# Performance work log

Hardware: AMD Instinct MI355X
Metric: run time of the kernel (lower is better)

## Reference

```python
import jax, jax.numpy as jnp
import numpy as np
import math

EPS = 1.1920929e-07  # torch.finfo(float32).eps, used by nn.RMSNorm(eps=None)

def rmsnorm(x, w):
    return x * jax.lax.rsqrt(jnp.mean(x * x, axis=-1, keepdims=True) + EPS) * w

def sinkhorn(logits, iters=20):
    m = jnp.exp(logits - logits.max(axis=-1, keepdims=True))
    def body(_, m):
        m = m / (m.sum(axis=-1, keepdims=True) + 1e-6)
        return m / (m.sum(axis=-2, keepdims=True) + 1e-6)
    return jax.lax.fori_loop(0, iters, body, m)

def ngram_hash(ids, mults):
    # ids [B,T] int32, mults [2,2,3] int32 -> [B,T,4]
    B, T = ids.shape
    padded = jnp.pad(ids, ((0, 0), (2, 0)))
    windows = jnp.stack([padded[:, k:k + T] for k in range(3)], axis=-1)  # [B,T,3]
    out = []
    for n_idx in range(2):
        L = n_idx + 2
        grams = windows[:, :, 3 - L:]                                     # [B,T,L]
        mixed = grams[:, :, None, :] * mults[n_idx, :, :L][None, None]    # [B,T,2,L]
        h = mixed[..., 0]
        for k in range(1, L):
            h = jnp.bitwise_xor(h, mixed[..., k])
        out.append(h % 4096)
    return jnp.concatenate(out, axis=2)

def short_conv(x, conv_w, norm_w):
    # depthwise causal conv, kernel 4: torch pads 3 both sides then slices [..., :T]
    B, T, G, C = x.shape
    xn = rmsnorm(x, norm_w).reshape(B, T, G * C).transpose(0, 2, 1)  # [B,GC,T]
    y = jax.lax.conv_general_dilated(xn, conv_w, (1,), [(3, 0)],
                                     feature_group_count=G * C,
                                     dimension_numbers=('NCH', 'OIH', 'NCH'))
    return jax.nn.silu(y).transpose(0, 2, 1).reshape(B, T, G, C)

def engram(x, ids, mults, emb_table, val_w, val_b, key_w, key_b, nq_w, nk_w, conv_w, convnorm_w):
    B, T = ids.shape
    hash_ids = ngram_hash(ids, mults) + jnp.array([0, 4096, 8192, 12288], dtype=jnp.int32)
    emb = emb_table[hash_ids].reshape(B, T, -1)                       # [B,T,256]
    v_base = emb @ val_w + val_b                                      # [B,T,128]
    k = rmsnorm(jnp.einsum('btd,sdc->btsc', emb, key_w) + key_b, nk_w)  # [B,T,4,128]
    q = rmsnorm(x, nq_w)
    gates = jax.nn.sigmoid(jnp.sum(q * k, axis=-1, keepdims=True) / math.sqrt(128.0))
    v_gated = v_base[:, :, None, :] * gates                           # [B,T,4,128]
    return v_gated + short_conv(v_gated, conv_w, convnorm_w)

def causal_attn(x, qkv_w, qkv_b, proj_w, proj_b):
    B, T, C = x.shape
    H, D = 4, C // 4
    q, k, v = jnp.split(x @ qkv_w + qkv_b, 3, axis=-1)
    q = q.reshape(B, T, H, D).transpose(0, 2, 1, 3)
    k = k.reshape(B, T, H, D).transpose(0, 2, 1, 3)
    v = v.reshape(B, T, H, D).transpose(0, 2, 1, 3)
    att = jnp.einsum('bhtd,bhsd->bhts', q, k) / math.sqrt(D)
    att = jnp.where(jnp.tril(jnp.ones((T, T), bool)), att, -jnp.inf)
    att = jax.nn.softmax(att, axis=-1)
    y = jnp.einsum('bhts,bhsd->bhtd', att, v).transpose(0, 2, 1, 3).reshape(B, T, C)
    return y @ proj_w + proj_b

def mhc(x, layer_fn, coef_w, pre_w, pre_b, post_w, post_b, res_w, res_b, a_pre, a_post, a_res, ln_w):
    B, T, n, C = x.shape
    xn = rmsnorm(x.reshape(B * T, n * C), coef_w)
    H_pre = jax.nn.sigmoid(a_pre * (xn @ pre_w + pre_b))             # [BT,n]
    H_post = 2.0 * jax.nn.sigmoid(a_post * (xn @ post_w + post_b))   # [BT,n]
    H_res = sinkhorn((a_res * (xn @ res_w + res_b)).reshape(-1, n, n))
    xp = x.reshape(B * T, n, C)
    x_agg = jnp.einsum('bn,bnc->bc', H_pre, xp)
    y = layer_fn(rmsnorm(x_agg.reshape(B, T, C), ln_w)).reshape(B * T, C)
    # faithful to torch einsum 'bjn,bc->bnc' applied to H_post.transpose(1,2) [BT,n,1]:
    # the stream dim j is CONTRACTED, leaving a size-1 dim that broadcasts over streams
    x_branch = H_post.sum(axis=-1)[:, None, None] * y[:, None, :]    # [BT,1,C]
    x_highway = jnp.einsum('bnm,bmc->bnc', H_res, xp)                # [BT,n,C]
    return (x_highway + x_branch).reshape(B, T, n, C)

def _forward(x, input_ids, eng_multipliers, eng_embedding, eng_val_w, eng_val_b, eng_key_w, eng_key_b, eng_nq_w, eng_nk_w, eng_conv_w, eng_convnorm_w, a_coef_w, a_pre_w, a_pre_b, a_post_w, a_post_b, a_res_w, a_res_b, a_alpha_pre, a_alpha_post, a_alpha_res, a_ln_w, qkv_w, qkv_b, attnproj_w, attnproj_b, m_coef_w, m_pre_w, m_pre_b, m_post_w, m_post_b, m_res_w, m_res_b, m_alpha_pre, m_alpha_post, m_alpha_res, m_ln_w, mlp_w1, mlp_b1, mlp_w2, mlp_b2):
    x = x + engram(x, input_ids, eng_multipliers, eng_embedding, eng_val_w, eng_val_b, eng_key_w, eng_key_b, eng_nq_w, eng_nk_w, eng_conv_w, eng_convnorm_w)
    attn_fn = lambda z: causal_attn(z, qkv_w, qkv_b, attnproj_w, attnproj_b)
    x = mhc(x, attn_fn, a_coef_w, a_pre_w, a_pre_b, a_post_w, a_post_b, a_res_w, a_res_b, a_alpha_pre, a_alpha_post, a_alpha_res, a_ln_w)
    mlp_fn = lambda z: jax.nn.silu(z @ mlp_w1 + mlp_b1) @ mlp_w2 + mlp_b2
    x = mhc(x, mlp_fn, m_coef_w, m_pre_w, m_pre_b, m_post_w, m_post_b, m_res_w, m_res_b, m_alpha_pre, m_alpha_post, m_alpha_res, m_ln_w)
    return x

def setup_inputs():
    key = jax.random.key(0)
    B, T = 256, 128
    def rnd(i, shp, scale=0.02):
        return jax.random.normal(jax.random.fold_in(key, i), shp, jnp.float32) * scale
    alpha = jnp.asarray(0.01, jnp.float32)
    return {
        'x': rnd(0, (B, T, 4, 128), 1.0),
        'input_ids': jax.random.randint(jax.random.fold_in(key, 1), (B, T), 0, 4096, jnp.int32),
        'eng_multipliers': jax.random.randint(jax.random.fold_in(key, 2), (2, 2, 3), 1, 10000, jnp.int32),
        'eng_embedding': rnd(3, (16384, 64)),
        'eng_val_w': rnd(4, (256, 128)), 'eng_val_b': jnp.zeros(128, jnp.float32),
        'eng_key_w': rnd(5, (4, 256, 128)), 'eng_key_b': jnp.zeros((4, 128), jnp.float32),
        'eng_nq_w': jnp.ones((4, 128), jnp.float32), 'eng_nk_w': jnp.ones((4, 128), jnp.float32),
        'eng_conv_w': rnd(6, (512, 1, 4), 0.1), 'eng_convnorm_w': jnp.ones((4, 128), jnp.float32),
        'a_coef_w': jnp.ones(512, jnp.float32),
        'a_pre_w': rnd(7, (512, 4)), 'a_pre_b': jnp.zeros(4, jnp.float32),
        'a_post_w': rnd(8, (512, 4)), 'a_post_b': jnp.zeros(4, jnp.float32),
        'a_res_w': rnd(9, (512, 16)), 'a_res_b': jnp.zeros(16, jnp.float32),
        'a_alpha_pre': alpha, 'a_alpha_post': alpha, 'a_alpha_res': alpha,
        'a_ln_w': jnp.ones(128, jnp.float32),
        'qkv_w': rnd(10, (128, 384)), 'qkv_b': jnp.zeros(384, jnp.float32),
        'attnproj_w': rnd(11, (128, 128)), 'attnproj_b': jnp.zeros(128, jnp.float32),
        'm_coef_w': jnp.ones(512, jnp.float32),
        'm_pre_w': rnd(12, (512, 4)), 'm_pre_b': jnp.zeros(4, jnp.float32),
        'm_post_w': rnd(13, (512, 4)), 'm_post_b': jnp.zeros(4, jnp.float32),
        'm_res_w': rnd(14, (512, 16)), 'm_res_b': jnp.zeros(16, jnp.float32),
        'm_alpha_pre': alpha, 'm_alpha_post': alpha, 'm_alpha_res': alpha,
        'm_ln_w': jnp.ones(128, jnp.float32),
        'mlp_w1': rnd(15, (128, 512)), 'mlp_b1': jnp.zeros(512, jnp.float32),
        'mlp_w2': rnd(16, (512, 128)), 'mlp_b2': jnp.zeros(128, jnp.float32),
    }

def reference(x, input_ids, eng_multipliers, eng_embedding, eng_val_w, eng_val_b, eng_key_w, eng_key_b, eng_nq_w, eng_nk_w, eng_conv_w, eng_convnorm_w, a_coef_w, a_pre_w, a_pre_b, a_post_w, a_post_b, a_res_w, a_res_b, a_alpha_pre, a_alpha_post, a_alpha_res, a_ln_w, qkv_w, qkv_b, attnproj_w, attnproj_b, m_coef_w, m_pre_w, m_pre_b, m_post_w, m_post_b, m_res_w, m_res_b, m_alpha_pre, m_alpha_post, m_alpha_res, m_ln_w, mlp_w1, mlp_b1, mlp_w2, mlp_b2):
    return _forward(x, input_ids, eng_multipliers, eng_embedding, eng_val_w, eng_val_b, eng_key_w, eng_key_b, eng_nq_w, eng_nk_w, eng_conv_w, eng_convnorm_w, a_coef_w, a_pre_w, a_pre_b, a_post_w, a_post_b, a_res_w, a_res_b, a_alpha_pre, a_alpha_post, a_alpha_res, a_ln_w, qkv_w, qkv_b, attnproj_w, attnproj_b, m_coef_w, m_pre_w, m_pre_b, m_post_w, m_post_b, m_res_w, m_res_b, m_alpha_pre, m_alpha_post, m_alpha_res, m_ln_w, mlp_w1, mlp_b1, mlp_w2, mlp_b2)
```

## Files before the change

### kernel.cpp

```cpp
#include <hip/hip_runtime.h>

#define BT 32768
#define TSEQ 128

constexpr float EPSF = 1.1920929e-07f;

typedef __attribute__((ext_vector_type(8))) short bf16x8;
typedef __attribute__((ext_vector_type(4))) float f32x4;

__device__ __forceinline__ float sigm(float z) { return 1.f / (1.f + __expf(-z)); }

__device__ __forceinline__ short bf16c(float f) {
  union { float f; unsigned u; } v; v.f = f;
  unsigned r = v.u + 0x7FFFu + ((v.u >> 16) & 1u);
  return (short)(r >> 16);
}
__device__ __forceinline__ float bf2f(short s) {
  union { unsigned u; float f; } v; v.u = ((unsigned)(unsigned short)s) << 16;
  return v.f;
}

__device__ __forceinline__ float red64(float v) {
  v += __shfl_xor(v, 1);  v += __shfl_xor(v, 2);  v += __shfl_xor(v, 4);
  v += __shfl_xor(v, 8);  v += __shfl_xor(v, 16); v += __shfl_xor(v, 32);
  return v;
}
__device__ __forceinline__ float red16(float v) {
  v += __shfl_xor(v, 1); v += __shfl_xor(v, 2); v += __shfl_xor(v, 4); v += __shfl_xor(v, 8);
  return v;
}
__device__ __forceinline__ float redmax16(float v) {
  v = fmaxf(v, __shfl_xor(v, 1)); v = fmaxf(v, __shfl_xor(v, 2));
  v = fmaxf(v, __shfl_xor(v, 4)); v = fmaxf(v, __shfl_xor(v, 8));
  return v;
}
__device__ __forceinline__ void load8(float* d, const float* p) {
  const float4 a = *reinterpret_cast<const float4*>(p);
  const float4 b = *reinterpret_cast<const float4*>(p + 4);
  d[0]=a.x; d[1]=a.y; d[2]=a.z; d[3]=a.w; d[4]=b.x; d[5]=b.y; d[6]=b.z; d[7]=b.w;
}

__global__ __launch_bounds__(256) void prep(
    const float* __restrict__ qkv_w, const float* __restrict__ proj_w,
    const float* __restrict__ mlp_w1, const float* __restrict__ mlp_w2,
    const float* __restrict__ val_w, const float* __restrict__ key_w,
    const float* __restrict__ a_res_w, const float* __restrict__ a_pre_w,
    const float* __restrict__ a_post_w,
    const float* __restrict__ m_res_w, const float* __restrict__ m_pre_w,
    const float* __restrict__ m_post_w,
    const float* __restrict__ a_res_b, const float* __restrict__ a_pre_b,
    const float* __restrict__ a_post_b,
    const float* __restrict__ m_res_b, const float* __restrict__ m_pre_b,
    const float* __restrict__ m_post_b,
    short* __restrict__ wt_qkv, short* __restrict__ wt_proj,
    short* __restrict__ wt_mlp1, short* __restrict__ wt_mlp2,
    short* __restrict__ wt_eng, short* __restrict__ wpk_a,
    short* __restrict__ wpk_m, float* __restrict__ bpk_a,
// ... 93 lines not shown
    for (int ks = 0; ks < 2; ++ks) {
      const int slot = ks * 4 + kg;
      bf16x8 af[2], bft;
#pragma unroll
      for (int mi = 0; mi < 2; ++mi) {
        const int r = wm * 32 + mi * 16 + lr;
        af[mi] = *reinterpret_cast<const bf16x8*>(&As[r * 64 + ((slot ^ (r & 7)) << 3)]);
      }
      {
        const int rb = wn * 16 + lr;
        bft = *reinterpret_cast<const bf16x8*>(&Bs[rb * 64 + ((slot ^ (rb & 7)) << 3)]);
      }
#pragma unroll
      for (int mi = 0; mi < 2; ++mi)
        acc[mi] = __builtin_amdgcn_mfma_f32_16x16x32_bf16(af[mi], bft, acc[mi], 0, 0, 0);
    }
  }
#pragma unroll
  for (int mi = 0; mi < 2; ++mi) {
    const int col = wn * 16 + lr;
    const float bv = bias[col];
#pragma unroll
    for (int j = 0; j < 4; ++j) {
      const int row = i0 + wm * 32 + mi * 16 + kg * 4 + j;
      out[(size_t)row * 32 + col] = acc[mi][j] + bv;
    }
  }
}

__global__ __launch_bounds__(256) void eng_mgemm(
    const int* __restrict__ ids, const int* __restrict__ mults,
    const float* __restrict__ table, const float* __restrict__ val_b,
    const short* __restrict__ wt_eng,
    float* __restrict__ vbase, float* __restrict__ kraw)
{
  __shared__ int hid[128][4];
  __shared__ short As[128 * 64];
  __shared__ short Bs[128 * 64];
  const int tid = threadIdx.x;
  const int i0 = blockIdx.x * 128;
  const int by = blockIdx.y;
  const int c0 = by * 128;
#pragma unroll
  for (int p = 0; p < 2; ++p) {
    const int idx = tid + p * 256;
    const int r = idx >> 2, wh = idx & 3;
    const int i = i0 + r;
    const int b = i >> 7, tt = i & 127;
    const int* __restrict__ row = ids + b * TSEQ;
    const int g2 = row[tt];
    const int g1 = (tt >= 1) ? row[tt - 1] : 0;
    const int g0 = (tt >= 2) ? row[tt - 2] : 0;
    int h;
    if (wh == 0)      h = ((g1 * mults[0]) ^ (g2 * mults[1])) & 4095;
    else if (wh == 1) h = (((g1 * mults[3]) ^ (g2 * mults[4])) & 4095) + 4096;
    else if (wh == 2) h = (((g0 * mults[6]) ^ (g1 * mults[7]) ^ (g2 * mults[8])) & 4095) + 8192;
    else              h = (((g0 * mults[9]) ^ (g1 * mults[10]) ^ (g2 * mults[11])) & 4095) + 12288;
    hid[r][wh] = h;
  }
  const int w = tid >> 6, l = tid & 63;
  const int wr = (w >> 1) * 64, wc = (w & 1) * 64;
  f32x4 acc[4][4];
#pragma unroll
  for (int mi = 0; mi < 4; ++mi)
#pragma unroll
    for (int ni = 0; ni < 4; ++ni) acc[mi][ni] = {0.f, 0.f, 0.f, 0.f};

// ... 22 lines not shown
#pragma unroll
    for (int ks = 0; ks < 2; ++ks) {
      const int slot = ks * 4 + kg;
      bf16x8 af[4], bft[4];
#pragma unroll
      for (int mi = 0; mi < 4; ++mi) {
        const int r = wr + mi * 16 + lr;
        af[mi] = *reinterpret_cast<const bf16x8*>(&As[r * 64 + ((slot ^ (r & 7)) << 3)]);
      }
#pragma unroll
      for (int ni = 0; ni < 4; ++ni) {
        const int r = wc + ni * 16 + lr;
        bft[ni] = *reinterpret_cast<const bf16x8*>(&Bs[r * 64 + ((slot ^ (r & 7)) << 3)]);
      }
#pragma unroll
      for (int mi = 0; mi < 4; ++mi)
#pragma unroll
        for (int ni = 0; ni < 4; ++ni)
          acc[mi][ni] = __builtin_amdgcn_mfma_f32_16x16x32_bf16(af[mi], bft[ni], acc[mi][ni], 0, 0, 0);
    }
  }
  const int lr = l & 15, hi = l >> 4;
#pragma unroll
  for (int mi = 0; mi < 4; ++mi)
#pragma unroll
    for (int ni = 0; ni < 4; ++ni) {
      const int col = wc + ni * 16 + lr;
#pragma unroll
      for (int j = 0; j < 4; ++j) {
        const int row = i0 + wr + mi * 16 + hi * 4 + j;
        if (by == 0)
          vbase[(size_t)row * 128 + col] = acc[mi][ni][j] + val_b[col];
        else
          kraw[(size_t)row * 512 + (by - 1) * 128 + col] = acc[mi][ni][j];
      }
    }
}

__global__ __launch_bounds__(512) void fused_gateconv(
    const float* __restrict__ kraw, const float* __restrict__ x,
    const float* __restrict__ vbase, const float* __restrict__ key_b,
    const float* __restrict__ nk_w, const float* __restrict__ nq_w,
    const float* __restrict__ conv_w, const float* __restrict__ cnw,
    float* __restrict__ xout, float* __restrict__ invout)
{
  __shared__ float vb[128 * 128];
  __shared__ float gA[128][4];
  __shared__ float gG[128][4];
  __shared__ float prt[128][2];
  const int tid = threadIdx.x;
  const size_t rowbase = (size_t)blockIdx.x * 128;
#pragma unroll
  for (int p = 0; p < 8; ++p) {
    const int idx = p * 512 + tid;
    *reinterpret_cast<float4*>(&vb[idx * 4]) =
        *reinterpret_cast<const float4*>(vbase + rowbase * 128 + (size_t)idx * 4);
  }
  __syncthreads();
  const int w = tid >> 6, l = tid & 63;
  {
    const int s = l >> 4, li = l & 15, c0 = li * 8, j0 = l * 8;
    float kb[8], nk[8], nq[8];
    load8(kb, key_b + s * 128 + c0);
    load8(nk, nk_w + s * 128 + c0);
    load8(nq, nq_w + s * 128 + c0);
    for (int it = 0; it < 16; ++it) {
      const int t = w * 16 + it;
      const size_t rg = rowbase + t;
      float kv[8], xv[8];
      load8(kv, kraw + rg * 512 + j0);
      load8(xv, x + rg * 512 + j0);
      float ssk = 0.f, ssx = 0.f;
#pragma unroll
      for (int jj = 0; jj < 8; ++jj) {
        kv[jj] += kb[jj];
        ssk = fmaf(kv[jj], kv[jj], ssk);
        ssx = fmaf(xv[jj], xv[jj], ssx);
      }
      ssk = red16(ssk);
      ssx = red16(ssx);
      const float invk = rsqrtf(ssk * (1.f / 128.f) + EPSF);
      const float invq = rsqrtf(ssx * (1.f / 128.f) + EPSF);
      float dot = 0.f;
#pragma unroll
      for (int jj = 0; jj < 8; ++jj)
        dot = fmaf(kv[jj] * invk * nk[jj], xv[jj] * invq * nq[jj], dot);
      dot = red16(dot);
      const float gate = sigm(dot * 0.08838834764831843f);
      const float2 vb2 = *reinterpret_cast<const float2*>(&vb[t * 128 + l * 2]);
      float ssv = vb2.x * vb2.x + vb2.y * vb2.y;
      ssv = red64(ssv);
      const float A = gate * rsqrtf(gate * gate * (ssv * (1.f / 128.f)) + EPSF);
      if (li == 0) { gG[t][s] = gate; gA[t][s] = A; }
    }
  }
  __syncthreads();
  {
    const int cg = tid >> 7;
    const int cjf = (tid & 127) * 4;
    const int cjh = cjf & 127;
    const int sj = cjf >> 7;
    float4 cwe[4];
#pragma unroll
    for (int e = 0; e < 4; ++e)
      cwe[e] = *reinterpret_cast<const float4*>(conv_w + (size_t)(cjf + e) * 4);
    const float4 cn4 = *reinterpret_cast<const float4*>(cnw + cjf);
    for (int tt = 0; tt < 32; ++tt) {
      const int t = tt * 4 + cg;
      float4 vbt[4]; float av[4];
#pragma unroll
      for (int kk = 0; kk < 4; ++kk) {
        const int t2 = t - 3 + kk;
        if (t2 >= 0) {
          vbt[kk] = *reinterpret_cast<const float4*>(&vb[t2 * 128 + cjh]);
          av[kk] = gA[t2][sj];
        } else {
          vbt[kk] = make_float4(0.f, 0.f, 0.f, 0.f);
          av[kk] = 0.f;
        }
      }
      float4 accv;
      accv.x = vbt[0].x*av[0]*cwe[0].x + vbt[1].x*av[1]*cwe[0].y + vbt[2].x*av[2]*cwe[0].z + vbt[3].x*av[3]*cwe[0].w;
      accv.y = vbt[0].y*av[0]*cwe[1].x + vbt[1].y*av[1]*cwe[1].y + vbt[2].y*av[2]*cwe[1].z + vbt[3].y*av[3]*cwe[1].w;
      accv.z = vbt[0].z*av[0]*cwe[2].x + vbt[1].z*av[1]*cwe[2].y + vbt[2].z*av[2]*cwe[2].z + vbt[3].z*av[3]*cwe[2].w;
      accv.w = vbt[0].w*av[0]*cwe[3].x + vbt[1].w*av[1]*cwe[3].y + vbt[2].w*av[2]*cwe[3].z + vbt[3].w*av[3]*cwe[3].w;
      const float4 x4 = *reinterpret_cast<const float4*>(x + (rowbase + t) * 512 + cjf);
      const float gg = gG[t][sj];
      float4 o;
      const float y0 = accv.x * cn4.x, y1 = accv.y * cn4.y;
      const float y2 = accv.z * cn4.z, y3 = accv.w * cn4.w;
      o.x = x4.x + vbt[3].x * gg + y0 * sigm(y0);
      o.y = x4.y + vbt[3].y * gg + y1 * sigm(y1);
      o.z = x4.z + vbt[3].z * gg + y2 * sigm(y2);
      o.w = x4.w + vbt[3].w * gg + y3 * sigm(y3);
      *reinterpret_cast<float4*>(xout + (rowbase + t) * 512 + cjf) = o;
      float ssq = o.x*o.x + o.y*o.y + o.z*o.z + o.w*o.w;
      ssq = red64(ssq);
      if (l == 0) prt[t][(tid >> 6) & 1] = ssq;
    }
  }
  __syncthreads();
  if (tid < 128)
    invout[rowbase + tid] = rsqrtf((prt[tid][0] + prt[tid][1]) * (1.f / 512.f) + EPSF);
}

__global__ __launch_bounds__(256) void mhc_sink2(
    const float* __restrict__ proj, const float* __restrict__ xin,
    const float* __restrict__ p_apre, const float* __restrict__ p_apost,
    const float* __restrict__ p_ares, const float* __restrict__ ln_w,
    unsigned short* __restrict__ xab, float* __restrict__ hres,
    float* __restrict__ hps)
{
  const int tid = threadIdx.x;
  const int l = tid & 63;
  const size_t i = (size_t)blockIdx.x * 4 + (tid >> 6);
  const float pv = proj[i * 32 + (l & 31)];
  const float apre = p_apre[0], apost = p_apost[0], ares = p_ares[0];
  const int n = l >> 4;
  const float hp = sigm(apre * __shfl(pv, 16 + n));
  float hsum = 0.f;
#pragma unroll
  for (int t2 = 0; t2 < 4; ++t2) hsum += 2.f * sigm(apost * __shfl(pv, 20 + t2));
  const float v = ares * pv;
  float rm = fmaxf(v, __shfl_xor(v, 1));
  rm = fmaxf(rm, __shfl_xor(rm, 2));
  float m = __expf(v - rm);
#pragma unroll
  for (int it = 0; it < 20; ++it) {
    float rs = m + __shfl_xor(m, 1);
    rs += __shfl_xor(rs, 2);
    m *= __builtin_amdgcn_rcpf(rs + 1e-6f);
    float cs = m + __shfl_xor(m, 4);
    cs += __shfl_xor(cs, 8);
    m *= __builtin_amdgcn_rcpf(cs + 1e-6f);
  }
  if (l < 16) hres[i * 16 + l] = m;
  if (l == 0) hps[i] = hsum;
  const int j0 = l * 8;
  float xv[8];
  load8(xv, xin + i * 512 + j0);
  float ag[8];
#pragma unroll
  for (int jj = 0; jj < 8; ++jj) {
    float a2 = hp * xv[jj];
    a2 += __shfl_xor(a2, 16);
    a2 += __shfl_xor(a2, 32);
    ag[jj] = a2;
  }
  float ssa = 0.f;
#pragma unroll
  for (int jj = 0; jj < 8; ++jj) ssa = fmaf(ag[jj], ag[jj], ssa);
  ssa = red16(ssa);
  const float inva = rsqrtf(ssa * (1.f / 128.f) + EPSF);
  if (l < 16) {
    float lnw[8];
    load8(lnw, ln_w + l * 8);
    bf16x8 o;
#pragma unroll
    for (int jj = 0; jj < 8; ++jj) o[jj] = bf16c(ag[jj] * inva * lnw[jj]);
    *reinterpret_cast<bf16x8*>(xab + i * 128 + l * 8) = o;
  }
}

template <int NT, int ACT>
__global__ __launch_bounds__(256) void mgemm_bf16A(
    const unsigned short* __restrict__ Ab, const short* __restrict__ WT,
    const float* __restrict__ bias, float* __restrict__ outp)
{
  __shared__ short As[128 * 64];
  __shared__ short Bs[128 * 64];
  const int tid = threadIdx.x;
  const int i0 = blockIdx.x * 128;
  const int c0 = blockIdx.y * 128;
  const int w = tid >> 6, l = tid & 63;
  const int wr = (w >> 1) * 64, wc = (w & 1) * 64;
  const int kg = l >> 4, lr = l & 15;
  f32x4 acc[4][4];
#pragma unroll
  for (int mi = 0; mi < 4; ++mi)
#pragma unroll
    for (int ni = 0; ni < 4; ++ni) acc[mi][ni] = {0.f, 0.f, 0.f, 0.f};

#pragma unroll
  for (int kc = 0; kc < 2; ++kc) {
    __syncthreads();
#pragma unroll
    for (int p = 0; p < 4; ++p) {
      const int idx = p * 256 + tid;
      const int r = idx >> 3, slb = idx & 7;
      const bf16x8 v = *reinterpret_cast<const bf16x8*>(Ab + (size_t)(i0 + r) * 128 + kc * 64 + slb * 8);
      *reinterpret_cast<bf16x8*>(&As[r * 64 + ((slb ^ (r & 7)) << 3)]) = v;
    }
#pragma unroll
    for (int p = 0; p < 4; ++p) {
      const int idx = p * 256 + tid;
      const int r = idx >> 3, slb = idx & 7;
      const bf16x8 v = *reinterpret_cast<const bf16x8*>(WT + (size_t)(c0 + r) * 128 + kc * 64 + slb * 8);
      *reinterpret_cast<bf16x8*>(&Bs[r * 64 + ((slb ^ (r & 7)) << 3)]) = v;
    }
    __syncthreads();
#pragma unroll
    for (int ks = 0; ks < 2; ++ks) {
      const int slot = ks * 4 + kg;
      bf16x8 af[4], bft[4];
#pragma unroll
      for (int mi = 0; mi < 4; ++mi) {
        const int r = wr + mi * 16 + lr;
        af[mi] = *reinterpret_cast<const bf16x8*>(&As[r * 64 + ((slot ^ (r & 7)) << 3)]);
      }
#pragma unroll
      for (int ni = 0; ni < 4; ++ni) {
        const int r = wc + ni * 16 + lr;
        bft[ni] = *reinterpret_cast<const bf16x8*>(&Bs[r * 64 + ((slot ^ (r & 7)) << 3)]);
      }
#pragma unroll
      for (int mi = 0; mi < 4; ++mi)
#pragma unroll
        for (int ni = 0; ni < 4; ++ni)
          acc[mi][ni] = __builtin_amdgcn_mfma_f32_16x16x32_bf16(af[mi], bft[ni], acc[mi][ni], 0, 0, 0);
    }
  }
#pragma unroll
  for (int mi = 0; mi < 4; ++mi)
#pragma unroll
    for (int ni = 0; ni < 4; ++ni) {
      const int col = c0 + wc + ni * 16 + lr;
      const float bv = bias[col];
#pragma unroll
      for (int j = 0; j < 4; ++j) {
        const int row = i0 + wr + mi * 16 + kg * 4 + j;
        float o = acc[mi][ni][j] + bv;
        if (ACT == 1) o = o * sigm(o);
        outp[(size_t)row * (NT * 128) + col] = o;
      }
    }
}

template <int KT, bool WITH_INV>
__global__ __launch_bounds__(512) void gemm_combine(
    const float* __restrict__ A, const int lda,
    const short* __restrict__ WT, const float* __restrict__ bias,
    const float* __restrict__ xst, const float* __restrict__ hres,
    const float* __restrict__ hps, float* __restrict__ outp,
    float* __restrict__ invout)
{
  __shared__ short As[128 * 64];
  __shared__ short Bs[128 * 64];
  __shared__ short yl[128 * 132];
  __shared__ float prt[128][2];
  const int tid = threadIdx.x;
  const size_t i0 = (size_t)blockIdx.x * 128;
  const int w = tid >> 6, l = tid & 63;
  const int wm = w >> 2, wn = w & 3;
  const int kg = l >> 4, lr = l & 15;
  f32x4 acc[4][2];
#pragma unroll
  for (int mi = 0; mi < 4; ++mi)
#pragma unroll
    for (int ni = 0; ni < 2; ++ni) acc[mi][ni] = {0.f, 0.f, 0.f, 0.f};
#pragma unroll
  for (int kc = 0; kc < KT; ++kc) {
    __syncthreads();
#pragma unroll
    for (int p = 0; p < 4; ++p) {
      const int idx = p * 512 + tid;
      const int r = idx >> 4, c4 = idx & 15;
      const float4 v = *reinterpret_cast<const float4*>(A + (i0 + r) * lda + kc * 64 + c4 * 4);
      short4 b4; b4.x = bf16c(v.x); b4.y = bf16c(v.y); b4.z = bf16c(v.z); b4.w = bf16c(v.w);
      *reinterpret_cast<short4*>(&As[r * 64 + (((c4 >> 1) ^ (r & 7)) << 3) + ((c4 & 1) << 2)]) = b4;
    }
#pragma unroll
    for (int p = 0; p < 2; ++p) {
      const int idx = p * 512 + tid;
      const int r = idx >> 3, slb = idx & 7;
      const bf16x8 v = *reinterpret_cast<const bf16x8*>(
          WT + (size_t)r * (KT * 64) + kc * 64 + slb * 8);
      *reinterpret_cast<bf16x8*>(&Bs[r * 64 + ((slb ^ (r & 7)) << 3)]) = v;
    }
    __syncthreads();
#pragma unroll
    for (int ks = 0; ks < 2; ++ks) {
      const int slot = ks * 4 + kg;
      bf16x8 af[4], bft[2];
#pragma unroll
      for (int mi = 0; mi < 4; ++mi) {
        const int r = wm * 64 + mi * 16 + lr;
        af[mi] = *reinterpret_cast<const bf16x8*>(&As[r * 64 + ((slot ^ (r & 7)) << 3)]);
      }
#pragma unroll
      for (int ni = 0; ni < 2; ++ni) {
        const int rb = wn * 32 + ni * 16 + lr;
        bft[ni] = *reinterpret_cast<const bf16x8*>(&Bs[rb * 64 + ((slot ^ (rb & 7)) << 3)]);
      }
#pragma unroll
      for (int mi = 0; mi < 4; ++mi)
#pragma unroll
        for (int ni = 0; ni < 2; ++ni)
          acc[mi][ni] = __builtin_amdgcn_mfma_f32_16x16x32_bf16(af[mi], bft[ni], acc[mi][ni], 0, 0, 0);
    }
  }
#pragma unroll
  for (int mi = 0; mi < 4; ++mi)
#pragma unroll
    for (int ni = 0; ni < 2; ++ni) {
      const int col = wn * 32 + ni * 16 + lr;
      const float bv = bias[col];
#pragma unroll
      for (int j = 0; j < 4; ++j) {
        const int row = wm * 64 + mi * 16 + kg * 4 + j;
        yl[row * 132 + col] = bf16c(acc[mi][ni][j] + bv);
      }
    }
  __syncthreads();
  const int c = tid & 127, tl = tid >> 7;
  for (int k = 0; k < 32; ++k) {
    const int t = tl * 32 + k;
    const size_t rg = i0 + t;
    float hv[16];
#pragma unroll
    for (int n16 = 0; n16 < 16; ++n16) hv[n16] = hres[rg * 16 + n16];
    const float g = hps[rg];
    const float yv = bf2f(yl[t * 132 + c]) * g;
    float xm[4];
#pragma unroll
    for (int m = 0; m < 4; ++m) xm[m] = xst[rg * 512 + m * 128 + c];
    float ssq = 0.f;
#pragma unroll
    for (int n = 0; n < 4; ++n) {
      const float o = hv[n*4+0]*xm[0] + hv[n*4+1]*xm[1] + hv[n*4+2]*xm[2] + hv[n*4+3]*xm[3] + yv;
      outp[rg * 512 + n * 128 + c] = o;
      if (WITH_INV) ssq = fmaf(o, o, ssq);
    }
    if (WITH_INV) {
      ssq = red64(ssq);
      if (l == 0) prt[t][(tid >> 6) & 1] = ssq;
    }
  }
  if (WITH_INV) {
    __syncthreads();
    if (tid < 128)
      invout[i0 + tid] = rsqrtf((prt[tid][0] + prt[tid][1]) * (1.f / 512.f) + EPSF);
  }
}

__global__ __launch_bounds__(256) void attn_mfma(
    const float* __restrict__ qkv, float* __restrict__ y)
{
  __shared__ short Ks[128 * 32];
  __shared__ short Vt[32 * 128];
  __shared__ short Ps[4][32 * 128];
  const int tid = threadIdx.x;
  const int b = blockIdx.x >> 2, h = blockIdx.x & 3;
  const float* __restrict__ base = qkv + (size_t)b * 128 * 384 + h * 32;
#pragma unroll
  for (int p = 0; p < 4; ++p) {
    const int idx = tid + p * 256;
    const int s = idx >> 3, c4 = idx & 7;
    const float4 v = *reinterpret_cast<const float4*>(base + (size_t)s * 384 + 128 + c4 * 4);
    short4 o; o.x = bf16c(v.x); o.y = bf16c(v.y); o.z = bf16c(v.z); o.w = bf16c(v.w);
    const int chunk = (c4 >> 1) ^ ((s >> 1) & 3);
    *reinterpret_cast<short4*>(&Ks[s * 32 + chunk * 8 + (c4 & 1) * 4]) = o;
  }
#pragma unroll
  for (int p = 0; p < 4; ++p) {
    const int idx = tid + p * 256;
    const int s = idx >> 3, c4 = idx & 7;
    const float4 v = *reinterpret_cast<const float4*>(base + (size_t)s * 384 + 256 + c4 * 4);
    const int schunk = s >> 3, soff = s & 7;
#pragma unroll
    for (int k = 0; k < 4; ++k) {
      const int d = c4 * 4 + k;
      const float vv = (k == 0) ? v.x : (k == 1) ? v.y : (k == 2) ? v.z : v.w;
      Vt[d * 128 + ((schunk ^ (d & 7)) << 3) + soff] = bf16c(vv);
    }
  }
  const int w = tid >> 6, l = tid & 63;
  const int g = l >> 4, lr = l & 15;
  bf16x8 qa[2];
#pragma unroll
  for (int mi = 0; mi < 2; ++mi) {
    const int row = w * 32 + mi * 16 + lr;
    const float* qp = base + (size_t)row * 384 + g * 8;
    const float4 a = *reinterpret_cast<const float4*>(qp);
    const float4 c = *reinterpret_cast<const float4*>(qp + 4);
    bf16x8 q;
    q[0] = bf16c(a.x); q[1] = bf16c(a.y); q[2] = bf16c(a.z); q[3] = bf16c(a.w);
    q[4] = bf16c(c.x); q[5] = bf16c(c.y); q[6] = bf16c(c.z); q[7] = bf16c(c.w);
    qa[mi] = q;
  }
  __syncthreads();
  const int ntmax = 2 * w + 1;
  bf16x8 ka[8];
#pragma unroll
  for (int nt = 0; nt < 8; ++nt)
    if (nt <= ntmax) {
      const int s = nt * 16 + lr;
      const int chunk = g ^ ((s >> 1) & 3);
      ka[nt] = *reinterpret_cast<const bf16x8*>(&Ks[s * 32 + chunk * 8]);
    }
  f32x4 sacc[2][8];
#pragma unroll
  for (int mi = 0; mi < 2; ++mi)
#pragma unroll
    for (int nt = 0; nt < 8; ++nt) sacc[mi][nt] = {0.f, 0.f, 0.f, 0.f};
#pragma unroll
  for (int mi = 0; mi < 2; ++mi)
#pragma unroll
    for (int nt = 0; nt < 8; ++nt)
      if (nt <= ntmax)
        sacc[mi][nt] = __builtin_amdgcn_mfma_f32_16x16x32_bf16(qa[mi], ka[nt], sacc[mi][nt], 0, 0, 0);
  const float scl = 0.17677669529663687f;
  float rv[2][4];
  short* const pw = Ps[w];
#pragma unroll
  for (int mi = 0; mi < 2; ++mi) {
#pragma unroll
    for (int j = 0; j < 4; ++j) {
      const int row = w * 32 + mi * 16 + g * 4 + j;
      float mx = -3.4e38f;
#pragma unroll
      for (int nt = 0; nt < 8; ++nt)
// ... 23 lines not shown
#pragma unroll
  for (int mi = 0; mi < 2; ++mi)
#pragma unroll
    for (int nt = 0; nt < 2; ++nt) oacc[mi][nt] = {0.f, 0.f, 0.f, 0.f};
#pragma unroll
  for (int kt = 0; kt < 4; ++kt)
    if (kt <= w) {
      bf16x8 pa[2], va[2];
#pragma unroll
      for (int mi = 0; mi < 2; ++mi) {
        const int rl = mi * 16 + lr;
        const int chunk = (4 * kt + g) ^ (rl & 7);
        pa[mi] = *reinterpret_cast<const bf16x8*>(&pw[rl * 128 + chunk * 8]);
      }
#pragma unroll
      for (int nt = 0; nt < 2; ++nt) {
        const int d = nt * 16 + lr;
        const int chunk = (4 * kt + g) ^ (d & 7);
        va[nt] = *reinterpret_cast<const bf16x8*>(&Vt[d * 128 + chunk * 8]);
      }
#pragma unroll
      for (int mi = 0; mi < 2; ++mi)
#pragma unroll
        for (int nt = 0; nt < 2; ++nt)
          oacc[mi][nt] = __builtin_amdgcn_mfma_f32_16x16x32_bf16(pa[mi], va[nt], oacc[mi][nt], 0, 0, 0);
    }
#pragma unroll
  for (int mi = 0; mi < 2; ++mi)
#pragma unroll
    for (int nt = 0; nt < 2; ++nt)
#pragma unroll
      for (int j = 0; j < 4; ++j) {
        const int row = w * 32 + mi * 16 + g * 4 + j;
        y[((size_t)b * 128 + row) * 128 + h * 32 + nt * 16 + lr] = oacc[mi][nt][j] * rv[mi][j];
      }
}

extern "C" void kernel_launch(void* const* d_in, const int* in_sizes, int n_in,
                              void* d_out, int out_size, void* d_ws, size_t ws_size,
                              hipStream_t stream)
{
  const float* x        = (const float*)d_in[0];
  const int*   ids      = (const int*)d_in[1];
  const int*   mults    = (const int*)d_in[2];
  const float* table    = (const float*)d_in[3];
  const float* val_w    = (const float*)d_in[4];
  const float* val_b    = (const float*)d_in[5];
  const float* key_w    = (const float*)d_in[6];
  const float* key_b    = (const float*)d_in[7];
  const float* nq_w     = (const float*)d_in[8];
  const float* nk_w     = (const float*)d_in[9];
  const float* conv_w   = (const float*)d_in[10];
  const float* cnw      = (const float*)d_in[11];
  const float* a_coef   = (const float*)d_in[12];
  const float* a_pre_w  = (const float*)d_in[13];
  const float* a_pre_b  = (const float*)d_in[14];
  const float* a_post_w = (const float*)d_in[15];
  const float* a_post_b = (const float*)d_in[16];
  const float* a_res_w  = (const float*)d_in[17];
  const float* a_res_b  = (const float*)d_in[18];
  const float* a_apre   = (const float*)d_in[19];
  const float* a_apost  = (const float*)d_in[20];
  const float* a_ares   = (const float*)d_in[21];
  const float* a_ln_w   = (const float*)d_in[22];
  const float* qkv_w    = (const float*)d_in[23];
  const float* qkv_b    = (const float*)d_in[24];
  const float* proj_w   = (const float*)d_in[25];
  const float* proj_b   = (const float*)d_in[26];
  const float* m_coef   = (const float*)d_in[27];
  const float* m_pre_w  = (const float*)d_in[28];
  const float* m_pre_b  = (const float*)d_in[29];
  const float* m_post_w = (const float*)d_in[30];
  const float* m_post_b = (const float*)d_in[31];
  const float* m_res_w  = (const float*)d_in[32];
  const float* m_res_b  = (const float*)d_in[33];
  const float* m_apre   = (const float*)d_in[34];
  const float* m_apost  = (const float*)d_in[35];
  const float* m_ares   = (const float*)d_in[36];
  const float* m_ln_w   = (const float*)d_in[37];
  const float* mlp_w1   = (const float*)d_in[38];
  const float* mlp_b1   = (const float*)d_in[39];
  const float* mlp_w2   = (const float*)d_in[40];
  const float* mlp_b2   = (const float*)d_in[41];

  float* out = (float*)d_out;
  float* ws  = (float*)d_ws;
  float* vbase = ws;
  float* kraw  = vbase + (size_t)BT * 128;
  float* y1    = kraw  + (size_t)BT * 512;
  float* hresb = y1    + (size_t)BT * 128;
  float* hpsb  = hresb + (size_t)BT * 16;
  float* inv1  = hpsb  + (size_t)BT;
  float* inv2  = inv1  + (size_t)BT;
  float* bpk_a = inv2  + (size_t)BT;
  float* bpk_m = bpk_a + 32;
  short* wt_qkv  = (short*)(bpk_m + 32);
  short* wt_proj = wt_qkv  + 49152;
  short* wt_mlp1 = wt_proj + 16384;
  short* wt_mlp2 = wt_mlp1 + 65536;
  short* wt_eng  = wt_mlp2 + 65536;
  short* wpk_a   = wt_eng  + 163840;
  short* wpk_m   = wpk_a   + 16384;
  unsigned short* xab = (unsigned short*)(wpk_m + 16384);
  float* proj24  = y1;

  prep<<<1537, 256, 0, stream>>>(qkv_w, proj_w, mlp_w1, mlp_w2, val_w, key_w,
                                 a_res_w, a_pre_w, a_post_w, m_res_w, m_pre_w, m_post_w,
                                 a_res_b, a_pre_b, a_post_b, m_res_b, m_pre_b, m_post_b,
                                 wt_qkv, wt_proj, wt_mlp1, wt_mlp2, wt_eng,
                                 wpk_a, wpk_m, bpk_a, bpk_m);

  eng_mgemm<<<dim3(BT / 128, 5), 256, 0, stream>>>(ids, mults, table, val_b, wt_eng,
                                                   vbase, kraw);
  fused_gateconv<<<256, 512, 0, stream>>>(kraw, x, vbase, key_b, nk_w, nq_w,
                                          conv_w, cnw, out, inv1);

  mgemm32<<<BT / 64, 256, 0, stream>>>(out, 512, wpk_a, bpk_a, proj24, 512, inv1, a_coef);
  mhc_sink2<<<BT / 4, 256, 0, stream>>>(proj24, out, a_apre, a_apost, a_ares, a_ln_w,
                                        xab, hresb, hpsb);
  mgemm_bf16A<3, 0><<<dim3(BT / 128, 3), 256, 0, stream>>>(xab, wt_qkv, qkv_b, kraw);
  attn_mfma<<<1024, 256, 0, stream>>>(kraw, y1);
  gemm_combine<2, true><<<256, 512, 0, stream>>>(y1, 128, wt_proj, proj_b,
                                                 out, hresb, hpsb, kraw, inv2);

  mgemm32<<<BT / 64, 256, 0, stream>>>(kraw, 512, wpk_m, bpk_m, proj24, 512, inv2, m_coef);
  mhc_sink2<<<BT / 4, 256, 0, stream>>>(proj24, kraw, m_apre, m_apost, m_ares, m_ln_w,
                                        xab, hresb, hpsb);
  mgemm_bf16A<4, 1><<<dim3(BT / 128, 4), 256, 0, stream>>>(xab, wt_mlp1, mlp_b1, out);
  gemm_combine<8, false><<<256, 512, 0, stream>>>(out, 512, wt_mlp2, mlp_b2,
                                                  kraw, hresb, hpsb, out, nullptr);

  (void)in_sizes; (void)n_in; (void)out_size; (void)ws_size;
}
```

Baseline: 313.9 us.

## Store intermediates as bf16 and shrink gateconv/combine tiles for more blocks

Intermediate activations (engram keys, qkv, attention output, MLP hidden) are now written as bf16 instead of fp32. Consumers load them directly without converting, which roughly halves the global memory traffic between kernels. fused_gateconv now processes 32 rows per block with a 3-row halo instead of 128 rows, and gemm_combine uses 64-row tiles, so both launch many more blocks. The trade-off is recomputing the gates on halo rows, extra rounding of keys to bf16 before the RMSNorm, and a rearranged workspace with aliased buffers.

```diff
diff --git a/kernel.cpp b/kernel.cpp
--- a/kernel.cpp
+++ b/kernel.cpp
@@ -23,6 +23,11 @@
 __device__ __forceinline__ float red64(float v) {
   v += __shfl_xor(v, 1);  v += __shfl_xor(v, 2);  v += __shfl_xor(v, 4);
   v += __shfl_xor(v, 8);  v += __shfl_xor(v, 16); v += __shfl_xor(v, 32);
+  return v;
+}
+__device__ __forceinline__ float red32(float v) {
+  v += __shfl_xor(v, 1); v += __shfl_xor(v, 2); v += __shfl_xor(v, 4);
+  v += __shfl_xor(v, 8); v += __shfl_xor(v, 16);
   return v;
 }
 __device__ __forceinline__ float red16(float v) {
@@ -182,7 +187,7 @@
     const int* __restrict__ ids, const int* __restrict__ mults,
     const float* __restrict__ table, const float* __restrict__ val_b,
     const short* __restrict__ wt_eng,
-    float* __restrict__ vbase, float* __restrict__ kraw)
+    float* __restrict__ vbase, unsigned short* __restrict__ krawb)
 {
   __shared__ int hid[128][4];
   __shared__ short As[128 * 64];
@@ -271,29 +276,35 @@
         if (by == 0)
           vbase[(size_t)row * 128 + col] = acc[mi][ni][j] + val_b[col];
         else
-          kraw[(size_t)row * 512 + (by - 1) * 128 + col] = acc[mi][ni][j];
-      }
-    }
-}
-
-__global__ __launch_bounds__(512) void fused_gateconv(
-    const float* __restrict__ kraw, const float* __restrict__ x,
+          krawb[(size_t)row * 512 + (by - 1) * 128 + col] =
+              (unsigned short)bf16c(acc[mi][ni][j]);
+      }
+    }
+}
+
+__global__ __launch_bounds__(256) void fused_gateconv(
+    const unsigned short* __restrict__ krawb, const float* __restrict__ x,
     const float* __restrict__ vbase, const float* __restrict__ key_b,
     const float* __restrict__ nk_w, const float* __restrict__ nq_w,
     const float* __restrict__ conv_w, const float* __restrict__ cnw,
     float* __restrict__ xout, float* __restrict__ invout)
 {
-  __shared__ float vb[128 * 128];
-  __shared__ float gA[128][4];
-  __shared__ float gG[128][4];
-  __shared__ float prt[128][2];
+  __shared__ float vb[35 * 128];
+  __shared__ float gA[35][4];
+  __shared__ float gG[35][4];
   const int tid = threadIdx.x;
-  const size_t rowbase = (size_t)blockIdx.x * 128;
-#pragma unroll
-  for (int p = 0; p < 8; ++p) {
-    const int idx = p * 512 + tid;
-    *reinterpret_cast<float4*>(&vb[idx * 4]) =
-        *reinterpret_cast<const float4*>(vbase + rowbase * 128 + (size_t)idx * 4);
+  const size_t rowbase = (size_t)blockIdx.x * 32;
+  const int tt0 = (int)(rowbase & 127);
+#pragma unroll
+  for (int p = 0; p < 5; ++p) {
+    const int idx = p * 256 + tid;
+    if (idx < 1120) {
+      const int hs = idx >> 5, c4 = (idx & 31) << 2;
+      float4 v = make_float4(0.f, 0.f, 0.f, 0.f);
+      if (tt0 - 3 + hs >= 0)
+        v = *reinterpret_cast<const float4*>(vbase + (rowbase - 3 + hs) * 128 + c4);
+      *reinterpret_cast<float4*>(&vb[hs * 128 + c4]) = v;
+    }
   }
   __syncthreads();
   const int w = tid >> 6, l = tid & 63;
@@ -303,11 +314,21 @@
     load8(kb, key_b + s * 128 + c0);
     load8(nk, nk_w + s * 128 + c0);
     load8(nq, nq_w + s * 128 + c0);
-    for (int it = 0; it < 16; ++it) {
-      const int t = w * 16 + it;
-      const size_t rg = rowbase + t;
+    for (int it = 0; it < 9; ++it) {
+      const int ht = it * 4 + w;
+      if (ht >= 35) break;
+      const int tt = tt0 - 3 + ht;
+      if (tt < 0) {
+        if (li == 0) { gG[ht][s] = 0.f; gA[ht][s] = 0.f; }
+        continue;
+      }
+      const size_t rg = rowbase - 3 + ht;
       float kv[8], xv[8];
-      load8(kv, kraw + rg * 512 + j0);
+      {
+        const bf16x8 kvb = *reinterpret_cast<const bf16x8*>(krawb + rg * 512 + j0);
+#pragma unroll
+        for (int jj = 0; jj < 8; ++jj) kv[jj] = bf2f(kvb[jj]);
+      }
       load8(xv, x + rg * 512 + j0);
       float ssk = 0.f, ssx = 0.f;
 #pragma unroll
@@ -326,61 +347,57 @@
         dot = fmaf(kv[jj] * invk * nk[jj], xv[jj] * invq * nq[jj], dot);
       dot = red16(dot);
       const float gate = sigm(dot * 0.08838834764831843f);
-      const float2 vb2 = *reinterpret_cast<const float2*>(&vb[t * 128 + l * 2]);
+      const float2 vb2 = *reinterpret_cast<const float2*>(&vb[ht * 128 + l * 2]);
       float ssv = vb2.x * vb2.x + vb2.y * vb2.y;
       ssv = red64(ssv);
       const float A = gate * rsqrtf(gate * gate * (ssv * (1.f / 128.f)) + EPSF);
-      if (li == 0) { gG[t][s] = gate; gA[t][s] = A; }
+      if (li == 0) { gG[ht][s] = gate; gA[ht][s] = A; }
     }
   }
   __syncthreads();
   {
-    const int cg = tid >> 7;
-    const int cjf = (tid & 127) * 4;
-    const int cjh = cjf & 127;
-    const int sj = cjf >> 7;
-    float4 cwe[4];
-#pragma unroll
-    for (int e = 0; e < 4; ++e)
-      cwe[e] = *reinterpret_cast<const float4*>(conv_w + (size_t)(cjf + e) * 4);
-    const float4 cn4 = *reinterpret_cast<const float4*>(cnw + cjf);
-    for (int tt = 0; tt < 32; ++tt) {
-      const int t = tt * 4 + cg;
-      float4 vbt[4]; float av[4];
-#pragma unroll
-      for (int kk = 0; kk < 4; ++kk) {
-        const int t2 = t - 3 + kk;
-        if (t2 >= 0) {
-          vbt[kk] = *reinterpret_cast<const float4*>(&vb[t2 * 128 + cjh]);
-          av[kk] = gA[t2][sj];
-        } else {
-          vbt[kk] = make_float4(0.f, 0.f, 0.f, 0.f);
-          av[kk] = 0.f;
+    const int tg = tid >> 5;
+    const int c4l = tid & 31;
+    const int cf = c4l * 4;
+    for (int ti = 0; ti < 4; ++ti) {
+      const int t = tg + ti * 8;
+      const size_t rg = rowbase + t;
+      float ssq = 0.f;
+#pragma unroll
+      for (int sj = 0; sj < 4; ++sj) {
+        const int j = sj * 128 + cf;
+        float4 cwe[4];
+#pragma unroll
+        for (int e = 0; e < 4; ++e)
+          cwe[e] = *reinterpret_cast<const float4*>(conv_w + (size_t)(j + e) * 4);
+        const float4 cn4 = *reinterpret_cast<const float4*>(cnw + j);
+        float4 vbt[4]; float av[4];
+#pragma unroll
+        for (int kk = 0; kk < 4; ++kk) {
+          vbt[kk] = *reinterpret_cast<const float4*>(&vb[(t + kk) * 128 + cf]);
+          av[kk] = gA[t + kk][sj];
         }
-      }
-      float4 accv;
-      accv.x = vbt[0].x*av[0]*cwe[0].x + vbt[1].x*av[1]*cwe[0].y + vbt[2].x*av[2]*cwe[0].z + vbt[3].x*av[3]*cwe[0].w;
-      accv.y = vbt[0].y*av[0]*cwe[1].x + vbt[1].y*av[1]*cwe[1].y + vbt[2].y*av[2]*cwe[1].z + vbt[3].y*av[3]*cwe[1].w;
-      accv.z = vbt[0].z*av[0]*cwe[2].x + vbt[1].z*av[1]*cwe[2].y + vbt[2].z*av[2]*cwe[2].z + vbt[3].z*av[3]*cwe[2].w;
-      accv.w = vbt[0].w*av[0]*cwe[3].x + vbt[1].w*av[1]*cwe[3].y + vbt[2].w*av[2]*cwe[3].z + vbt[3].w*av[3]*cwe[3].w;
-      const float4 x4 = *reinterpret_cast<const float4*>(x + (rowbase + t) * 512 + cjf);
-      const float gg = gG[t][sj];
-      float4 o;
-      const float y0 = accv.x * cn4.x, y1 = accv.y * cn4.y;
-      const float y2 = accv.z * cn4.z, y3 = accv.w * cn4.w;
-      o.x = x4.x + vbt[3].x * gg + y0 * sigm(y0);
-      o.y = x4.y + vbt[3].y * gg + y1 * sigm(y1);
-      o.z = x4.z + vbt[3].z * gg + y2 * sigm(y2);
-      o.w = x4.w + vbt[3].w * gg + y3 * sigm(y3);
-      *reinterpret_cast<float4*>(xout + (rowbase + t) * 512 + cjf) = o;
-      float ssq = o.x*o.x + o.y*o.y + o.z*o.z + o.w*o.w;
-      ssq = red64(ssq);
-      if (l == 0) prt[t][(tid >> 6) & 1] = ssq;
-    }
-  }
-  __syncthreads();
-  if (tid < 128)
-    invout[rowbase + tid] = rsqrtf((prt[tid][0] + prt[tid][1]) * (1.f / 512.f) + EPSF);
+        const float gg = gG[t + 3][sj];
+        float4 accv;
+        accv.x = vbt[0].x*av[0]*cwe[0].x + vbt[1].x*av[1]*cwe[0].y + vbt[2].x*av[2]*cwe[0].z + vbt[3].x*av[3]*cwe[0].w;
+        accv.y = vbt[0].y*av[0]*cwe[1].x + vbt[1].y*av[1]*cwe[1].y + vbt[2].y*av[2]*cwe[1].z + vbt[3].y*av[3]*cwe[1].w;
+        accv.z = vbt[0].z*av[0]*cwe[2].x + vbt[1].z*av[1]*cwe[2].y + vbt[2].z*av[2]*cwe[2].z + vbt[3].z*av[3]*cwe[2].w;
+        accv.w = vbt[0].w*av[0]*cwe[3].x + vbt[1].w*av[1]*cwe[3].y + vbt[2].w*av[2]*cwe[3].z + vbt[3].w*av[3]*cwe[3].w;
+        const float4 x4 = *reinterpret_cast<const float4*>(x + rg * 512 + j);
+        const float y0 = accv.x * cn4.x, y1 = accv.y * cn4.y;
+        const float y2 = accv.z * cn4.z, y3 = accv.w * cn4.w;
+        float4 o;
+        o.x = x4.x + vbt[3].x * gg + y0 * sigm(y0);
+        o.y = x4.y + vbt[3].y * gg + y1 * sigm(y1);
+        o.z = x4.z + vbt[3].z * gg + y2 * sigm(y2);
+        o.w = x4.w + vbt[3].w * gg + y3 * sigm(y3);
+        *reinterpret_cast<float4*>(xout + rg * 512 + j) = o;
+        ssq += o.x*o.x + o.y*o.y + o.z*o.z + o.w*o.w;
+      }
+      ssq = red32(ssq);
+      if (c4l == 0) invout[rg] = rsqrtf(ssq * (1.f / 512.f) + EPSF);
+    }
+  }
 }
 
 __global__ __launch_bounds__(256) void mhc_sink2(
@@ -444,7 +461,7 @@
 template <int NT, int ACT>
 __global__ __launch_bounds__(256) void mgemm_bf16A(
     const unsigned short* __restrict__ Ab, const short* __restrict__ WT,
-    const float* __restrict__ bias, float* __restrict__ outp)
+    const float* __restrict__ bias, unsigned short* __restrict__ outp)
 {
   __shared__ short As[128 * 64];
   __shared__ short Bs[128 * 64];
@@ -510,43 +527,40 @@
         const int row = i0 + wr + mi * 16 + kg * 4 + j;
         float o = acc[mi][ni][j] + bv;
         if (ACT == 1) o = o * sigm(o);
-        outp[(size_t)row * (NT * 128) + col] = o;
+        outp[(size_t)row * (NT * 128) + col] = (unsigned short)bf16c(o);
       }
     }
 }
 
 template <int KT, bool WITH_INV>
 __global__ __launch_bounds__(512) void gemm_combine(
-    const float* __restrict__ A, const int lda,
+    const unsigned short* __restrict__ Ab, const int lda,
     const short* __restrict__ WT, const float* __restrict__ bias,
     const float* __restrict__ xst, const float* __restrict__ hres,
     const float* __restrict__ hps, float* __restrict__ outp,
     float* __restrict__ invout)
 {
-  __shared__ short As[128 * 64];
+  __shared__ short As[64 * 64];
   __shared__ short Bs[128 * 64];
-  __shared__ short yl[128 * 132];
-  __shared__ float prt[128][2];
+  __shared__ short yl[64 * 132];
+  __shared__ float prt[64][2];
   const int tid = threadIdx.x;
-  const size_t i0 = (size_t)blockIdx.x * 128;
+  const size_t i0 = (size_t)blockIdx.x * 64;
   const int w = tid >> 6, l = tid & 63;
   const int wm = w >> 2, wn = w & 3;
   const int kg = l >> 4, lr = l & 15;
-  f32x4 acc[4][2];
-#pragma unroll
-  for (int mi = 0; mi < 4; ++mi)
+  f32x4 acc[2][2];
+#pragma unroll
+  for (int mi = 0; mi < 2; ++mi)
 #pragma unroll
     for (int ni = 0; ni < 2; ++ni) acc[mi][ni] = {0.f, 0.f, 0.f, 0.f};
 #pragma unroll
   for (int kc = 0; kc < KT; ++kc) {
     __syncthreads();
-#pragma unroll
-    for (int p = 0; p < 4; ++p) {
-      const int idx = p * 512 + tid;
-      const int r = idx >> 4, c4 = idx & 15;
-      const float4 v = *reinterpret_cast<const float4*>(A + (i0 + r) * lda + kc * 64 + c4 * 4);
-      short4 b4; b4.x = bf16c(v.x); b4.y = bf16c(v.y); b4.z = bf16c(v.z); b4.w = bf16c(v.w);
-      *reinterpret_cast<short4*>(&As[r * 64 + (((c4 >> 1) ^ (r & 7)) << 3) + ((c4 & 1) << 2)]) = b4;
+    {
+      const int r = tid >> 3, slb = tid & 7;
+      const bf16x8 v = *reinterpret_cast<const bf16x8*>(Ab + (i0 + r) * lda + kc * 64 + slb * 8);
+      *reinterpret_cast<bf16x8*>(&As[r * 64 + ((slb ^ (r & 7)) << 3)]) = v;
     }
 #pragma unroll
     for (int p = 0; p < 2; ++p) {
@@ -560,10 +574,10 @@
 #pragma unroll
     for (int ks = 0; ks < 2; ++ks) {
       const int slot = ks * 4 + kg;
-      bf16x8 af[4], bft[2];
-#pragma unroll
-      for (int mi = 0; mi < 4; ++mi) {
-        const int r = wm * 64 + mi * 16 + lr;
+      bf16x8 af[2], bft[2];
+#pragma unroll
+      for (int mi = 0; mi < 2; ++mi) {
+        const int r = wm * 32 + mi * 16 + lr;
         af[mi] = *reinterpret_cast<const bf16x8*>(&As[r * 64 + ((slot ^ (r & 7)) << 3)]);
       }
 #pragma unroll
@@ -572,28 +586,28 @@
         bft[ni] = *reinterpret_cast<const bf16x8*>(&Bs[rb * 64 + ((slot ^ (rb & 7)) << 3)]);
       }
 #pragma unroll
-      for (int mi = 0; mi < 4; ++mi)
+      for (int mi = 0; mi < 2; ++mi)
 #pragma unroll
         for (int ni = 0; ni < 2; ++ni)
           acc[mi][ni] = __builtin_amdgcn_mfma_f32_16x16x32_bf16(af[mi], bft[ni], acc[mi][ni], 0, 0, 0);
     }
   }
 #pragma unroll
-  for (int mi = 0; mi < 4; ++mi)
+  for (int mi = 0; mi < 2; ++mi)
 #pragma unroll
     for (int ni = 0; ni < 2; ++ni) {
       const int col = wn * 32 + ni * 16 + lr;
       const float bv = bias[col];
 #pragma unroll
       for (int j = 0; j < 4; ++j) {
-        const int row = wm * 64 + mi * 16 + kg * 4 + j;
+        const int row = wm * 32 + mi * 16 + kg * 4 + j;
         yl[row * 132 + col] = bf16c(acc[mi][ni][j] + bv);
       }
     }
   __syncthreads();
   const int c = tid & 127, tl = tid >> 7;
-  for (int k = 0; k < 32; ++k) {
-    const int t = tl * 32 + k;
+  for (int k = 0; k < 16; ++k) {
+    const int t = tl * 16 + k;
     const size_t rg = i0 + t;
     float hv[16];
 #pragma unroll
@@ -617,40 +631,39 @@
   }
   if (WITH_INV) {
     __syncthreads();
-    if (tid < 128)
+    if (tid < 64)
       invout[i0 + tid] = rsqrtf((prt[tid][0] + prt[tid][1]) * (1.f / 512.f) + EPSF);
   }
 }
 
 __global__ __launch_bounds__(256) void attn_mfma(
-    const float* __restrict__ qkv, float* __restrict__ y)
+    const unsigned short* __restrict__ qkv, unsigned short* __restrict__ y)
 {
   __shared__ short Ks[128 * 32];
   __shared__ short Vt[32 * 128];
   __shared__ short Ps[4][32 * 128];
   const int tid = threadIdx.x;
   const int b = blockIdx.x >> 2, h = blockIdx.x & 3;
-  const float* __restrict__ base = qkv + (size_t)b * 128 * 384 + h * 32;
+  const unsigned short* __restrict__ base = qkv + (size_t)b * 128 * 384 + h * 32;
+#pragma unroll
+  for (int p = 0; p < 2; ++p) {
+    const int idx = tid + p * 256;
+    const int s = idx >> 2, c8 = idx & 3;
+    const bf16x8 v = *reinterpret_cast<const bf16x8*>(base + (size_t)s * 384 + 128 + c8 * 8);
+    const int chunk = c8 ^ ((s >> 1) & 3);
+    *reinterpret_cast<bf16x8*>(&Ks[s * 32 + chunk * 8]) = v;
+  }
 #pragma unroll
   for (int p = 0; p < 4; ++p) {
     const int idx = tid + p * 256;
     const int s = idx >> 3, c4 = idx & 7;
-    const float4 v = *reinterpret_cast<const float4*>(base + (size_t)s * 384 + 128 + c4 * 4);
-    short4 o; o.x = bf16c(v.x); o.y = bf16c(v.y); o.z = bf16c(v.z); o.w = bf16c(v.w);
-    const int chunk = (c4 >> 1) ^ ((s >> 1) & 3);
-    *reinterpret_cast<short4*>(&Ks[s * 32 + chunk * 8 + (c4 & 1) * 4]) = o;
-  }
-#pragma unroll
-  for (int p = 0; p < 4; ++p) {
-    const int idx = tid + p * 256;
-    const int s = idx >> 3, c4 = idx & 7;
-    const float4 v = *reinterpret_cast<const float4*>(base + (size_t)s * 384 + 256 + c4 * 4);
+    const ushort4 v = *reinterpret_cast<const ushort4*>(base + (size_t)s * 384 + 256 + c4 * 4);
     const int schunk = s >> 3, soff = s & 7;
 #pragma unroll
     for (int k = 0; k < 4; ++k) {
       const int d = c4 * 4 + k;
-      const float vv = (k == 0) ? v.x : (k == 1) ? v.y : (k == 2) ? v.z : v.w;
-      Vt[d * 128 + ((schunk ^ (d & 7)) << 3) + soff] = bf16c(vv);
+      const unsigned short vv = (k == 0) ? v.x : (k == 1) ? v.y : (k == 2) ? v.z : v.w;
+      Vt[d * 128 + ((schunk ^ (d & 7)) << 3) + soff] = (short)vv;
     }
   }
   const int w = tid >> 6, l = tid & 63;
@@ -659,13 +672,7 @@
 #pragma unroll
   for (int mi = 0; mi < 2; ++mi) {
     const int row = w * 32 + mi * 16 + lr;
-    const float* qp = base + (size_t)row * 384 + g * 8;
-    const float4 a = *reinterpret_cast<const float4*>(qp);
-    const float4 c = *reinterpret_cast<const float4*>(qp + 4);
-    bf16x8 q;
-    q[0] = bf16c(a.x); q[1] = bf16c(a.y); q[2] = bf16c(a.z); q[3] = bf16c(a.w);
-    q[4] = bf16c(c.x); q[5] = bf16c(c.y); q[6] = bf16c(c.z); q[7] = bf16c(c.w);
-    qa[mi] = q;
+    qa[mi] = *reinterpret_cast<const bf16x8*>(base + (size_t)row * 384 + g * 8);
   }
   __syncthreads();
   const int ntmax = 2 * w + 1;
@@ -755,7 +762,8 @@
 #pragma unroll
       for (int j = 0; j < 4; ++j) {
         const int row = w * 32 + mi * 16 + g * 4 + j;
-        y[((size_t)b * 128 + row) * 128 + h * 32 + nt * 16 + lr] = oacc[mi][nt][j] * rv[mi][j];
+        y[((size_t)b * 128 + row) * 128 + h * 32 + nt * 16 + lr] =
+            (unsigned short)bf16c(oacc[mi][nt][j] * rv[mi][j]);
       }
 }
 
@@ -808,15 +816,15 @@
 
   float* out = (float*)d_out;
   float* ws  = (float*)d_ws;
-  float* vbase = ws;
-  float* kraw  = vbase + (size_t)BT * 128;
-  float* y1    = kraw  + (size_t)BT * 512;
-  float* hresb = y1    + (size_t)BT * 128;
-  float* hpsb  = hresb + (size_t)BT * 16;
-  float* inv1  = hpsb  + (size_t)BT;
-  float* inv2  = inv1  + (size_t)BT;
-  float* bpk_a = inv2  + (size_t)BT;
-  float* bpk_m = bpk_a + 32;
+  float* x2     = ws;
+  float* vbase  = ws;
+  float* proj24 = x2 + (size_t)BT * 512;
+  float* hresb  = proj24 + (size_t)BT * 32;
+  float* hpsb   = hresb + (size_t)BT * 16;
+  float* inv1   = hpsb + (size_t)BT;
+  float* inv2   = inv1 + (size_t)BT;
+  float* bpk_a  = inv2 + (size_t)BT;
+  float* bpk_m  = bpk_a + 32;
   short* wt_qkv  = (short*)(bpk_m + 32);
   short* wt_proj = wt_qkv  + 49152;
   short* wt_mlp1 = wt_proj + 16384;
@@ -825,7 +833,8 @@
   short* wpk_a   = wt_eng  + 163840;
   short* wpk_m   = wpk_a   + 16384;
   unsigned short* xab = (unsigned short*)(wpk_m + 16384);
-  float* proj24  = y1;
+  unsigned short* big = xab + (size_t)BT * 128;
+  unsigned short* y1b = big + (size_t)BT * 512;
 
   prep<<<1537, 256, 0, stream>>>(qkv_w, proj_w, mlp_w1, mlp_w2, val_w, key_w,
                                  a_res_w, a_pre_w, a_post_w, m_res_w, m_pre_w, m_post_w,
@@ -834,24 +843,24 @@
                                  wpk_a, wpk_m, bpk_a, bpk_m);
 
   eng_mgemm<<<dim3(BT / 128, 5), 256, 0, stream>>>(ids, mults, table, val_b, wt_eng,
-                                                   vbase, kraw);
-  fused_gateconv<<<256, 512, 0, stream>>>(kraw, x, vbase, key_b, nk_w, nq_w,
-                                          conv_w, cnw, out, inv1);
+                                                   vbase, big);
+  fused_gateconv<<<BT / 32, 256, 0, stream>>>(big, x, vbase, key_b, nk_w, nq_w,
+                                              conv_w, cnw, out, inv1);
 
   mgemm32<<<BT / 64, 256, 0, stream>>>(out, 512, wpk_a, bpk_a, proj24, 512, inv1, a_coef);
   mhc_sink2<<<BT / 4, 256, 0, stream>>>(proj24, out, a_apre, a_apost, a_ares, a_ln_w,
                                         xab, hresb, hpsb);
-  mgemm_bf16A<3, 0><<<dim3(BT / 128, 3), 256, 0, stream>>>(xab, wt_qkv, qkv_b, kraw);
-  attn_mfma<<<1024, 256, 0, stream>>>(kraw, y1);
-  gemm_combine<2, true><<<256, 512, 0, stream>>>(y1, 128, wt_proj, proj_b,
-                                                 out, hresb, hpsb, kraw, inv2);
-
-  mgemm32<<<BT / 64, 256, 0, stream>>>(kraw, 512, wpk_m, bpk_m, proj24, 512, inv2, m_coef);
-  mhc_sink2<<<BT / 4, 256, 0, stream>>>(proj24, kraw, m_apre, m_apost, m_ares, m_ln_w,
+  mgemm_bf16A<3, 0><<<dim3(BT / 128, 3), 256, 0, stream>>>(xab, wt_qkv, qkv_b, big);
+  attn_mfma<<<1024, 256, 0, stream>>>(big, y1b);
+  gemm_combine<2, true><<<BT / 64, 512, 0, stream>>>(y1b, 128, wt_proj, proj_b,
+                                                     out, hresb, hpsb, x2, inv2);
+
+  mgemm32<<<BT / 64, 256, 0, stream>>>(x2, 512, wpk_m, bpk_m, proj24, 512, inv2, m_coef);
+  mhc_sink2<<<BT / 4, 256, 0, stream>>>(proj24, x2, m_apre, m_apost, m_ares, m_ln_w,
                                         xab, hresb, hpsb);
-  mgemm_bf16A<4, 1><<<dim3(BT / 128, 4), 256, 0, stream>>>(xab, wt_mlp1, mlp_b1, out);
-  gemm_combine<8, false><<<256, 512, 0, stream>>>(out, 512, wt_mlp2, mlp_b2,
-                                                  kraw, hresb, hpsb, out, nullptr);
+  mgemm_bf16A<4, 1><<<dim3(BT / 128, 4), 256, 0, stream>>>(xab, wt_mlp1, mlp_b1, big);
+  gemm_combine<8, false><<<BT / 64, 512, 0, stream>>>(big, 512, wt_mlp2, mlp_b2,
+                                                      x2, hresb, hpsb, out, nullptr);
 
   (void)in_sizes; (void)n_in; (void)out_size; (void)ws_size;
 }
```

New measurement: 306.5 us. 2.4% less time.
